# Kernel optimization log

Hardware: AMD Instinct MI355X
Metric: run time of the kernel (lower is better)

The kernel has to match this reference:

```python
import jax, jax.numpy as jnp
import numpy as np

N, E, IN_DIM, HID = 50000, 800000, 512, 256
EPS = 1e-5


def _gat_layer(x, W, a_src, a_dst, b, src, dst, n, heads, ch):
    # x: [N, F_in] -> h: [N, H, C]
    h = (x @ W).reshape(n, heads, ch)
    alpha_src = jnp.sum(h * a_src, axis=-1)  # [N, H]
    alpha_dst = jnp.sum(h * a_dst, axis=-1)  # [N, H]
    e = jax.nn.leaky_relu(alpha_src[src] + alpha_dst[dst], negative_slope=0.2)  # [E', H]
    # segment softmax over incoming edges of each destination node
    m = jax.ops.segment_max(e, dst, num_segments=n)  # [N, H]
    ex = jnp.exp(e - m[dst])
    den = jax.ops.segment_sum(ex, dst, num_segments=n)  # [N, H]
    alpha = ex / den[dst]
    out = jax.ops.segment_sum(alpha[:, :, None] * h[src], dst, num_segments=n)  # [N, H, C]
    return out.reshape(n, heads * ch) + b


def _layer_norm(x, w, b):
    mu = jnp.mean(x, axis=-1, keepdims=True)
    var = jnp.mean(jnp.square(x - mu), axis=-1, keepdims=True)
    return (x - mu) * jax.lax.rsqrt(var + EPS) * w + b


def setup_inputs() -> dict:
    key = jax.random.key(0)
    ks = jax.random.split(key, 16)
    d = {}
    d['x'] = jax.random.normal(ks[0], (N, IN_DIM), dtype=jnp.float32)
    d['edge_index'] = jax.random.randint(ks[1], (2, E), 0, N, dtype=jnp.int32)
    s = 0.05
    # layer 0: GATConv(512, 64, heads=4)
    d['W0'] = jax.random.normal(ks[2], (IN_DIM, HID), dtype=jnp.float32) * s
    d['as0'] = jax.random.normal(ks[3], (4, 64), dtype=jnp.float32) * s
    d['ad0'] = jax.random.normal(ks[4], (4, 64), dtype=jnp.float32) * s
    d['b0'] = jnp.zeros((HID,), dtype=jnp.float32)
    d['lnw0'] = jnp.ones((HID,), dtype=jnp.float32)
    d['lnb0'] = jnp.zeros((HID,), dtype=jnp.float32)
    # layer 1: GATConv(256, 64, heads=4)
    d['W1'] = jax.random.normal(ks[5], (HID, HID), dtype=jnp.float32) * s
    d['as1'] = jax.random.normal(ks[6], (4, 64), dtype=jnp.float32) * s
    d['ad1'] = jax.random.normal(ks[7], (4, 64), dtype=jnp.float32) * s
    d['b1'] = jnp.zeros((HID,), dtype=jnp.float32)
    d['lnw1'] = jnp.ones((HID,), dtype=jnp.float32)
    d['lnb1'] = jnp.zeros((HID,), dtype=jnp.float32)
    # layer 2: GATConv(256, 256, heads=1)
    d['W2'] = jax.random.normal(ks[8], (HID, HID), dtype=jnp.float32) * s
    d['as2'] = jax.random.normal(ks[9], (1, HID), dtype=jnp.float32) * s
    d['ad2'] = jax.random.normal(ks[10], (1, HID), dtype=jnp.float32) * s
    d['b2'] = jnp.zeros((HID,), dtype=jnp.float32)
    d['lnw2'] = jnp.ones((HID,), dtype=jnp.float32)
    d['lnb2'] = jnp.zeros((HID,), dtype=jnp.float32)
    return d


def reference(x, edge_index, W0, as0, ad0, b0, lnw0, lnb0,
              W1, as1, ad1, b1, lnw1, lnb1,
              W2, as2, ad2, b2, lnw2, lnb2):
    n = x.shape[0]
    loop = jnp.arange(n, dtype=edge_index.dtype)
    src = jnp.concatenate([edge_index[0], loop])  # PyG add_self_loops=True
    dst = jnp.concatenate([edge_index[1], loop])
    h = _gat_layer(x, W0, as0, ad0, b0, src, dst, n, 4, 64)
    h = jax.nn.elu(_layer_norm(h, lnw0, lnb0))
    h = _gat_layer(h, W1, as1, ad1, b1, src, dst, n, 4, 64)
    h = jax.nn.elu(_layer_norm(h, lnw1, lnb1))
    h = _gat_layer(h, W2, as2, ad2, b2, src, dst, n, 1, HID)
    h = jax.nn.elu(_layer_norm(h, lnw2, lnb2))
    return h
```

## Files before the change

kernel.cpp:

```cpp
#include <hip/hip_runtime.h>

#define HID 256
#define EPSV 1e-5f
#define ASTR 72
#define BSTR 40

typedef __bf16 bf16x8 __attribute__((ext_vector_type(8)));
typedef float  floatx4 __attribute__((ext_vector_type(4)));

static __device__ __forceinline__ ushort f2bf(float f) {
  union { float f; unsigned int i; } c; c.f = f;
  unsigned int u = c.i;
  u += 0x7FFFu + ((u >> 16) & 1u);
  return (ushort)(u >> 16);
}
static __device__ __forceinline__ float bf2f(ushort u) {
  union { unsigned int i; float f; } c; c.i = ((unsigned int)u) << 16; return c.f;
}

__global__ void count_kernel(const int* __restrict__ ei, int* __restrict__ deg, int E, int tot) {
  int i = blockIdx.x * blockDim.x + threadIdx.x;
  if (i < tot) {
    int dst = (i < E) ? ei[E + i] : (i - E);
    atomicAdd(&deg[dst], 1);
  }
}

__global__ void scanA_kernel(const int* __restrict__ deg, int* __restrict__ incl,
                             int* __restrict__ sums, int n) {
  __shared__ int buf[1024];
  const int t = threadIdx.x;
  const int i = blockIdx.x * 1024 + t;
  int x = (i < n) ? deg[i] : 0;
  buf[t] = x;
  __syncthreads();
  for (int off = 1; off < 1024; off <<= 1) {
    int v = (t >= off) ? buf[t - off] : 0;
    __syncthreads();
    buf[t] += v;
    __syncthreads();
  }
  if (i < n) incl[i] = buf[t];
  if (t == 1023) sums[blockIdx.x] = buf[1023];
}

__global__ void scanB_kernel(int* __restrict__ sums, int* __restrict__ offs, int nblk) {
  __shared__ int buf[256];
  const int t = threadIdx.x;
  int x = (t < nblk) ? sums[t] : 0;
  buf[t] = x;
  __syncthreads();
  for (int off = 1; off < 256; off <<= 1) {
    int v = (t >= off) ? buf[t - off] : 0;
    __syncthreads();
    buf[t] += v;
    __syncthreads();
  }
  if (t < nblk) offs[t] = buf[t] - x;
  if (t == nblk) offs[nblk] = buf[nblk - 1];
}

__global__ void scanC_kernel(const int* __restrict__ deg, const int* __restrict__ incl,
                             const int* __restrict__ offs, int* __restrict__ rp,
                             int* __restrict__ cur, int n, int nblk) {
  const int i = blockIdx.x * 1024 + threadIdx.x;
  if (i < n) {
    int v = offs[blockIdx.x] + incl[i] - deg[i];
    rp[i] = v;
    cur[i] = v;
  }
  if (i == 0) rp[n] = offs[nblk];
}

__global__ void scatter_kernel(const int* __restrict__ ei, int* __restrict__ cur,
                               int* __restrict__ csr, int E, int tot) {
  int i = blockIdx.x * blockDim.x + threadIdx.x;
  if (i < tot) {
    int src = (i < E) ? ei[i] : (i - E);
    int dst = (i < E) ? ei[E + i] : (i - E);
    int pos = atomicAdd(&cur[dst], 1);
    csr[pos] = src;
  }
}

__global__ void transpose_kernel(const float* __restrict__ W, ushort* __restrict__ Wt, int K) {
  int i = blockIdx.x * blockDim.x + threadIdx.x;
  if (i < K * 256) {
    int k = i >> 8, m = i & 255;
    Wt[m * K + k] = f2bf(W[i]);
  }
}

__global__ __launch_bounds__(256) void gemm_kernel(
    const float* __restrict__ A, const ushort* __restrict__ Bt,
    ushort* __restrict__ hb, int nrows, int K) {
  __shared__ ushort At[128 * ASTR];
  __shared__ ushort Bs[128 * BSTR];
  const int tid  = threadIdx.x;
  const int lane = tid & 63;
  const int wave = tid >> 6;
  const int quad = lane >> 4;
  const int m16  = lane & 15;
  const int row0 = blockIdx.x * 128;
  const int col0 = blockIdx.y * 128;
  const int wm = (wave >> 1) * 64;
  const int wn = (wave & 1) * 64;

  floatx4 acc[4][4];
  #pragma unroll
  for (int i = 0; i < 4; i++)
    #pragma unroll
    for (int j = 0; j < 4; j++) acc[i][j] = (floatx4){0.f, 0.f, 0.f, 0.f};

  const int arow = tid >> 3;
  const int acol = (tid & 7) * 4;
  const int brow = tid >> 2;
  const int bcol = (tid & 3) * 8;

  for (int k0 = 0; k0 < K; k0 += 32) {
    #pragma unroll
    for (int i = 0; i < 4; i++) {
      int r = arow + 32 * i;
      int ar = min(row0 + r, nrows - 1);
      floatx4 v = *(const floatx4*)(A + (size_t)ar * K + k0 + acol);
      union { ushort us[4]; unsigned long long u64; } ph, pl;
      #pragma unroll
      for (int j = 0; j < 4; j++) {
        ushort hi = f2bf(v[j]);
        ph.us[j] = hi;
        pl.us[j] = f2bf(v[j] - bf2f(hi));
      }
      *(unsigned long long*)&At[r * ASTR + acol]      = ph.u64;
      *(unsigned long long*)&At[r * ASTR + 32 + acol] = pl.u64;
    }
    #pragma unroll
    for (int i = 0; i < 2; i++) {
      int r = brow + 64 * i;
      *(int4*)&Bs[r * BSTR + bcol] =
          *(const int4*)(Bt + (size_t)(col0 + r) * K + k0 + bcol);
    }
    __syncthreads();
    bf16x8 bfr[4];
    #pragma unroll
    for (int j = 0; j < 4; j++)
      bfr[j] = *(const bf16x8*)&Bs[(wn + j * 16 + m16) * BSTR + quad * 8];
    #pragma unroll
    for (int p = 0; p < 2; p++) {
      bf16x8 af[4];
      #pragma unroll
      for (int i = 0; i < 4; i++)
        af[i] = *(const bf16x8*)&At[(wm + i * 16 + m16) * ASTR + p * 32 + quad * 8];
      #pragma unroll
      for (int i = 0; i < 4; i++)
        #pragma unroll
        for (int j = 0; j < 4; j++)
          acc[i][j] = __builtin_amdgcn_mfma_f32_16x16x32_bf16(af[i], bfr[j], acc[i][j], 0, 0, 0);
    }
    __syncthreads();
  }
  #pragma unroll
  for (int i = 0; i < 4; i++) {
    int rbase = row0 + wm + i * 16 + quad * 4;
    #pragma unroll
    for (int j = 0; j < 4; j++) {
      int col = col0 + wn + j * 16 + m16;
      #pragma unroll
      for (int r = 0; r < 4; r++) {
        int row = rbase + r;
        if (row < nrows) hb[(size_t)row * HID + col] = f2bf(acc[i][j][r]);
      }
    }
  }
}

__global__ __launch_bounds__(256) void gemm_packed_kernel(
    const ushort* __restrict__ A, const ushort* __restrict__ Bt,
    ushort* __restrict__ hb, int nrows) {
  __shared__ ushort At[128 * BSTR];
  __shared__ ushort Bs[128 * BSTR];
  const int tid  = threadIdx.x;
  const int lane = tid & 63;
  const int wave = tid >> 6;
  const int quad = lane >> 4;
  const int m16  = lane & 15;
  const int row0 = blockIdx.x * 128;
  const int col0 = blockIdx.y * 128;
  const int wm = (wave >> 1) * 64;
  const int wn = (wave & 1) * 64;

  floatx4 acc[4][4];
  #pragma unroll
  for (int i = 0; i < 4; i++)
    #pragma unroll
    for (int j = 0; j < 4; j++) acc[i][j] = (floatx4){0.f, 0.f, 0.f, 0.f};

  const int srow = tid >> 2;
  const int scol = (tid & 3) * 8;

  for (int k0 = 0; k0 < 512; k0 += 32) {
    const int kb = k0 & 255;
    #pragma unroll
    for (int i = 0; i < 2; i++) {
      int r = srow + 64 * i;
      int ar = min(row0 + r, nrows - 1);
      *(int4*)&At[r * BSTR + scol] = *(const int4*)(A + (size_t)ar * 512 + k0 + scol);
      *(int4*)&Bs[r * BSTR + scol] = *(const int4*)(Bt + (size_t)(col0 + r) * 256 + kb + scol);
    }
    __syncthreads();
    bf16x8 af[4], bfr[4];
    #pragma unroll
    for (int j = 0; j < 4; j++)
      bfr[j] = *(const bf16x8*)&Bs[(wn + j * 16 + m16) * BSTR + quad * 8];
    #pragma unroll
    for (int i = 0; i < 4; i++)
      af[i] = *(const bf16x8*)&At[(wm + i * 16 + m16) * BSTR + quad * 8];
    #pragma unroll
    for (int i = 0; i < 4; i++)
      #pragma unroll
      for (int j = 0; j < 4; j++)
        acc[i][j] = __builtin_amdgcn_mfma_f32_16x16x32_bf16(af[i], bfr[j], acc[i][j], 0, 0, 0);
    __syncthreads();
  }
  #pragma unroll
  for (int i = 0; i < 4; i++) {
    int rbase = row0 + wm + i * 16 + quad * 4;
    #pragma unroll
    for (int j = 0; j < 4; j++) {
      int col = col0 + wn + j * 16 + m16;
      #pragma unroll
      for (int r = 0; r < 4; r++) {
        int row = rbase + r;
        if (row < nrows) hb[(size_t)row * HID + col] = f2bf(acc[i][j][r]);
      }
    }
  }
}

__global__ __launch_bounds__(256) void alpha_kernel(
    const ushort* __restrict__ hb, const float* __restrict__ avs,
    const float* __restrict__ avd, float* __restrict__ asrc,
    float* __restrict__ adst, int H, int n) {
  const int t = threadIdx.x, w = t >> 6, lane = t & 63;
  const int nid = blockIdx.x * 4 + w;
  if (nid >= n) return;
  const int ch = 4 * lane;
  uint2 hv = *(const uint2*)(hb + (size_t)nid * HID + ch);
  float h0 = __uint_as_float(hv.x << 16);
  float h1 = __uint_as_float(hv.x & 0xffff0000u);
  float h2 = __uint_as_float(hv.y << 16);
  float h3 = __uint_as_float(hv.y & 0xffff0000u);
  floatx4 vs = *(const floatx4*)(avs + ch);
  floatx4 vd = *(const floatx4*)(avd + ch);
  float s = h0 * vs[0] + h1 * vs[1] + h2 * vs[2] + h3 * vs[3];
  float d = h0 * vd[0] + h1 * vd[1] + h2 * vd[2] + h3 * vd[3];
  #pragma unroll
  for (int o = 1; o < 16; o <<= 1) { s += __shfl_xor(s, o); d += __shfl_xor(d, o); }
  if (H == 4) {
    if ((lane & 15) == 0) {
      int hh = lane >> 4;
      asrc[nid * 4 + hh] = s;
      adst[nid * 4 + hh] = d;
    }
  } else {
    s += __shfl_xor(s, 16); d += __shfl_xor(d, 16);
    s += __shfl_xor(s, 32); d += __shfl_xor(d, 32);
    if (lane == 0) { asrc[nid] = s; adst[nid] = d; }
  }
}

__global__ __launch_bounds__(256) void agg_ln_kernel(
    const ushort* __restrict__ hb, const float* __restrict__ asrc,
    const float* __restrict__ adst, const int* __restrict__ rp,
    const int* __restrict__ csr,
    const float* __restrict__ bias, const float* __restrict__ lnw,
    const float* __restrict__ lnb, ushort* __restrict__ apk,
    float* __restrict__ fout, int H, int n) {
  __shared__ float2 exs[4][64];
  const int t = threadIdx.x;
  const int w = t >> 6, lane = t & 63;
  const int nid = blockIdx.x * 4 + w;
  if (nid >= n) return;
  const int CH = (H == 4) ? 16 : 64;
  const int jj = lane & (CH - 1);
  const int hh = (H == 4) ? (lane >> 4) : 0;
  const int ch = 4 * lane;
  const float ad = adst[nid * H + hh];
  const int beg = rp[nid], end = rp[nid + 1];
  const char* hbase = (const char*)hb + ch * 2;
  float den = 0.f;
  float a0 = 0.f, a1 = 0.f, a2 = 0.f, a3 = 0.f;
  float b0 = 0.f, b1 = 0.f, b2 = 0.f, b3 = 0.f;

  for (int c0 = beg; c0 < end; c0 += CH) {
    const int cnt = min(CH, end - c0);
    int s = (lane < cnt) ? csr[c0 + lane] : 0;
    s = __shfl(s, jj);
    float ex = 0.f;
    if (jj < cnt) {
      float e = asrc[s * H + hh] + ad;
      e = (e > 0.f) ? e : 0.2f * e;
      ex = __expf(fminf(e, 60.f));
    }
    exs[w][lane] = make_float2(ex, __int_as_float(s << 9));
    float dsum = ex;
    #pragma unroll
    for (int o = 32; o > 0; o >>= 1)
      if (o < CH) dsum += __shfl_xor(dsum, o);
    den += dsum;
    const float2* exw = &exs[w][hh * CH];
    int j = 0;
    for (; j + 2 <= cnt; j += 2) {
      float2 q0 = exw[j];
      float2 q1 = exw[j + 1];
      uint2 u0 = *(const uint2*)(hbase + __float_as_int(q0.y));
      uint2 u1 = *(const uint2*)(hbase + __float_as_int(q1.y));
      a0 = fmaf(q0.x, __uint_as_float(u0.x << 16), a0);
      a1 = fmaf(q0.x, __uint_as_float(u0.x & 0xffff0000u), a1);
      a2 = fmaf(q0.x, __uint_as_float(u0.y << 16), a2);
      a3 = fmaf(q0.x, __uint_as_float(u0.y & 0xffff0000u), a3);
      b0 = fmaf(q1.x, __uint_as_float(u1.x << 16), b0);
      b1 = fmaf(q1.x, __uint_as_float(u1.x & 0xffff0000u), b1);
      b2 = fmaf(q1.x, __uint_as_float(u1.y << 16), b2);
      b3 = fmaf(q1.x, __uint_as_float(u1.y & 0xffff0000u), b3);
    }
    if (j < cnt) {
      float2 q0 = exw[j];
      uint2 u0 = *(const uint2*)(hbase + __float_as_int(q0.y));
      a0 = fmaf(q0.x, __uint_as_float(u0.x << 16), a0);
      a1 = fmaf(q0.x, __uint_as_float(u0.x & 0xffff0000u), a1);
      a2 = fmaf(q0.x, __uint_as_float(u0.y << 16), a2);
      a3 = fmaf(q0.x, __uint_as_float(u0.y & 0xffff0000u), a3);
    }
  }
  a0 += b0; a1 += b1; a2 += b2; a3 += b3;

  const float inv = 1.f / den;
  const floatx4 bia = *(const floatx4*)(bias + ch);
  float v0 = a0 * inv + bia[0];
  float v1 = a1 * inv + bia[1];
  float v2 = a2 * inv + bia[2];
  float v3 = a3 * inv + bia[3];
  float r1 = v0 + v1 + v2 + v3;
  #pragma unroll
  for (int o = 32; o > 0; o >>= 1) r1 += __shfl_xor(r1, o);
  float mu = r1 * (1.f / HID);
  float d0 = v0 - mu, d1 = v1 - mu, d2 = v2 - mu, d3 = v3 - mu;
  float r2 = d0 * d0 + d1 * d1 + d2 * d2 + d3 * d3;
  #pragma unroll
  for (int o = 32; o > 0; o >>= 1) r2 += __shfl_xor(r2, o);
  float rstd = rsqrtf(r2 * (1.f / HID) + EPSV);
  const floatx4 wv = *(const floatx4*)(lnw + ch);
  const floatx4 bv = *(const floatx4*)(lnb + ch);
  float y0 = d0 * rstd * wv[0] + bv[0];
  float y1 = d1 * rstd * wv[1] + bv[1];
  float y2 = d2 * rstd * wv[2] + bv[2];
  float y3 = d3 * rstd * wv[3] + bv[3];
  float o0 = (y0 > 0.f) ? y0 : expm1f(y0);
  float o1 = (y1 > 0.f) ? y1 : expm1f(y1);
  float o2 = (y2 > 0.f) ? y2 : expm1f(y2);
  float o3 = (y3 > 0.f) ? y3 : expm1f(y3);
  if (apk) {
    union { ushort us[4]; unsigned long long u64; } ph, pl;
    ushort h0 = f2bf(o0), h1 = f2bf(o1), h2 = f2bf(o2), h3 = f2bf(o3);
    ph.us[0] = h0; ph.us[1] = h1; ph.us[2] = h2; ph.us[3] = h3;
    pl.us[0] = f2bf(o0 - bf2f(h0)); pl.us[1] = f2bf(o1 - bf2f(h1));
    pl.us[2] = f2bf(o2 - bf2f(h2)); pl.us[3] = f2bf(o3 - bf2f(h3));
    *(unsigned long long*)(apk + (size_t)nid * 512 + ch)       = ph.u64;
    *(unsigned long long*)(apk + (size_t)nid * 512 + 256 + ch) = pl.u64;
  } else {
    floatx4 ov; ov[0] = o0; ov[1] = o1; ov[2] = o2; ov[3] = o3;
    *(floatx4*)(fout + (size_t)nid * HID + ch) = ov;
  }
}

extern "C" void kernel_launch(void* const* d_in, const int* in_sizes, int n_in,
                              void* d_out, int out_size, void* d_ws, size_t ws_size,
                              hipStream_t stream) {
  const float* x  = (const float*)d_in[0];
  const int*   ei = (const int*)d_in[1];
  const float* Wm[3]  = {(const float*)d_in[2], (const float*)d_in[8],  (const float*)d_in[14]};
  const float* Avs[3] = {(const float*)d_in[3], (const float*)d_in[9],  (const float*)d_in[15]};
  const float* Avd[3] = {(const float*)d_in[4], (const float*)d_in[10], (const float*)d_in[16]};
  const float* Bia[3] = {(const float*)d_in[5], (const float*)d_in[11], (const float*)d_in[17]};
  const float* Lnw[3] = {(const float*)d_in[6], (const float*)d_in[12], (const float*)d_in[18]};
  const float* Lnb[3] = {(const float*)d_in[7], (const float*)d_in[13], (const float*)d_in[19]};
  const int n = in_sizes[0] / 512;
  const int E = in_sizes[1] / 2;
  const int tot = E + n;
  const int nblk = (n + 1023) / 1024;

  char* p = (char*)d_ws;
  ushort* hb   = (ushort*)p; p += (size_t)n * HID * 2;
  ushort* apk  = (ushort*)p; p += (size_t)n * 512 * 2;
  ushort* Wt   = (ushort*)p; p += 256 * 512 * 2;
  float*  asrc = (float*)p;  p += (size_t)n * 4 * 4;
  float*  adst = (float*)p;  p += (size_t)n * 4 * 4;
  int* rp   = (int*)p; p += (size_t)(n + 1) * 4;
  int* cur  = (int*)p; p += (size_t)n * 4;
  int* csr  = (int*)p; p += (size_t)tot * 4;
  int* deg  = (int*)p; p += (size_t)n * 4;
  int* incl = (int*)p; p += (size_t)n * 4;
  int* sums = (int*)p; p += (size_t)(nblk + 1) * 4;
  int* offs = (int*)p; p += (size_t)(nblk + 1) * 4;

  hipMemsetAsync(deg, 0, (size_t)n * 4, stream);
  count_kernel<<<(tot + 255) / 256, 256, 0, stream>>>(ei, deg, E, tot);
  scanA_kernel<<<nblk, 1024, 0, stream>>>(deg, incl, sums, n);
  scanB_kernel<<<1, 256, 0, stream>>>(sums, offs, nblk);
  scanC_kernel<<<nblk, 1024, 0, stream>>>(deg, incl, offs, rp, cur, n, nblk);
  scatter_kernel<<<(tot + 255) / 256, 256, 0, stream>>>(ei, cur, csr, E, tot);

  const int KB[3] = {512, 256, 256};
  const int HH[3] = {4, 4, 1};
  dim3 gg((n + 127) / 128, 2);
  for (int l = 0; l < 3; l++) {
    transpose_kernel<<<(KB[l] * 256 + 255) / 256, 256, 0, stream>>>(Wm[l], Wt, KB[l]);
    if (l == 0)
      gemm_kernel<<<gg, 256, 0, stream>>>(x, Wt, hb, n, 512);
    else
      gemm_packed_kernel<<<gg, 256, 0, stream>>>(apk, Wt, hb, n);
    alpha_kernel<<<(n + 3) / 4, 256, 0, stream>>>(hb, Avs[l], Avd[l], asrc, adst, HH[l], n);
    agg_ln_kernel<<<(n + 3) / 4, 256, 0, stream>>>(
        hb, asrc, adst, rp, csr, Bia[l], Lnw[l], Lnb[l],
        (l < 2) ? apk : (ushort*)nullptr,
        (l == 2) ? (float*)d_out : (float*)nullptr, HH[l], n);
  }
}
```

Before: 640.1 us.

## Fuse attention-logit computation into GEMM epilogue and prefetch/unroll aggregation

Removes the separate alpha kernel by computing per-row source and destination attention logits from the fp32 GEMM accumulators in an epilogue. Heads are reduced with lane shuffles, and the single-head layer combines its partial sums with atomics into zeroed buffers. The aggregation kernel also prefetches the next chunk of CSR indices and unrolls the gather loop four-wide with more independent accumulators. This saves a launch and a re-read of the bf16 features, and the logits now come from unrounded values. In exchange it adds atomics, extra memsets and more register pressure.

Result: no change. 641.7 us (+0.2%).

```diff
diff --git a/kernel.cpp b/kernel.cpp
--- a/kernel.cpp
+++ b/kernel.cpp
@@ -91,9 +91,50 @@
   }
 }
 
+static __device__ __forceinline__ void alpha_epilogue(
+    const floatx4 (&acc)[4][4], const float* __restrict__ avs,
+    const float* __restrict__ avd, float* __restrict__ asrc,
+    float* __restrict__ adst, int row0, int col0, int wm, int wn,
+    int quad, int m16, int H, int nrows) {
+  float sv[4], dv[4];
+  #pragma unroll
+  for (int j = 0; j < 4; j++) {
+    int col = col0 + wn + j * 16 + m16;
+    sv[j] = avs[col];
+    dv[j] = avd[col];
+  }
+  const int hd = (col0 + wn) >> 6;
+  #pragma unroll
+  for (int i = 0; i < 4; i++) {
+    #pragma unroll
+    for (int r = 0; r < 4; r++) {
+      int row = row0 + wm + i * 16 + quad * 4 + r;
+      float s = 0.f, d = 0.f;
+      #pragma unroll
+      for (int j = 0; j < 4; j++) {
+        s = fmaf(acc[i][j][r], sv[j], s);
+        d = fmaf(acc[i][j][r], dv[j], d);
+      }
+      #pragma unroll
+      for (int o = 1; o < 16; o <<= 1) { s += __shfl_xor(s, o); d += __shfl_xor(d, o); }
+      if (m16 == 0 && row < nrows) {
+        if (H == 4) {
+          asrc[row * 4 + hd] = s;
+          adst[row * 4 + hd] = d;
+        } else {
+          atomicAdd(&asrc[row], s);
+          atomicAdd(&adst[row], d);
+        }
+      }
+    }
+  }
+}
+
 __global__ __launch_bounds__(256) void gemm_kernel(
     const float* __restrict__ A, const ushort* __restrict__ Bt,
-    ushort* __restrict__ hb, int nrows, int K) {
+    ushort* __restrict__ hb, const float* __restrict__ avs,
+    const float* __restrict__ avd, float* __restrict__ asrc,
+    float* __restrict__ adst, int nrows, int K) {
   __shared__ ushort At[128 * ASTR];
   __shared__ ushort Bs[128 * BSTR];
   const int tid  = threadIdx.x;
@@ -171,11 +212,14 @@
       }
     }
   }
+  alpha_epilogue(acc, avs, avd, asrc, adst, row0, col0, wm, wn, quad, m16, 4, nrows);
 }
 
 __global__ __launch_bounds__(256) void gemm_packed_kernel(
     const ushort* __restrict__ A, const ushort* __restrict__ Bt,
-    ushort* __restrict__ hb, int nrows) {
+    ushort* __restrict__ hb, const float* __restrict__ avs,
+    const float* __restrict__ avd, float* __restrict__ asrc,
+    float* __restrict__ adst, int nrows, int H) {
   __shared__ ushort At[128 * BSTR];
   __shared__ ushort Bs[128 * BSTR];
   const int tid  = threadIdx.x;
@@ -234,38 +278,7 @@
       }
     }
   }
-}
-
-__global__ __launch_bounds__(256) void alpha_kernel(
-    const ushort* __restrict__ hb, const float* __restrict__ avs,
-    const float* __restrict__ avd, float* __restrict__ asrc,
-    float* __restrict__ adst, int H, int n) {
-  const int t = threadIdx.x, w = t >> 6, lane = t & 63;
-  const int nid = blockIdx.x * 4 + w;
-  if (nid >= n) return;
-  const int ch = 4 * lane;
-  uint2 hv = *(const uint2*)(hb + (size_t)nid * HID + ch);
-  float h0 = __uint_as_float(hv.x << 16);
-  float h1 = __uint_as_float(hv.x & 0xffff0000u);
-  float h2 = __uint_as_float(hv.y << 16);
-  float h3 = __uint_as_float(hv.y & 0xffff0000u);
-  floatx4 vs = *(const floatx4*)(avs + ch);
-  floatx4 vd = *(const floatx4*)(avd + ch);
-  float s = h0 * vs[0] + h1 * vs[1] + h2 * vs[2] + h3 * vs[3];
-  float d = h0 * vd[0] + h1 * vd[1] + h2 * vd[2] + h3 * vd[3];
-  #pragma unroll
-  for (int o = 1; o < 16; o <<= 1) { s += __shfl_xor(s, o); d += __shfl_xor(d, o); }
-  if (H == 4) {
-    if ((lane & 15) == 0) {
-      int hh = lane >> 4;
-      asrc[nid * 4 + hh] = s;
-      adst[nid * 4 + hh] = d;
-    }
-  } else {
-    s += __shfl_xor(s, 16); d += __shfl_xor(d, 16);
-    s += __shfl_xor(s, 32); d += __shfl_xor(d, 32);
-    if (lane == 0) { asrc[nid] = s; adst[nid] = d; }
-  }
+  alpha_epilogue(acc, avs, avd, asrc, adst, row0, col0, wm, wn, quad, m16, H, nrows);
 }
 
 __global__ __launch_bounds__(256) void agg_ln_kernel(
@@ -290,10 +303,23 @@
   float den = 0.f;
   float a0 = 0.f, a1 = 0.f, a2 = 0.f, a3 = 0.f;
   float b0 = 0.f, b1 = 0.f, b2 = 0.f, b3 = 0.f;
+  float c0_ = 0.f, c1 = 0.f, c2 = 0.f, c3 = 0.f;
+  float d0_ = 0.f, d1 = 0.f, d2 = 0.f, d3 = 0.f;
+
+  int snext = 0;
+  {
+    int cnt0 = min(CH, end - beg);
+    if (lane < cnt0) snext = csr[beg + lane];
+  }
 
   for (int c0 = beg; c0 < end; c0 += CH) {
     const int cnt = min(CH, end - c0);
-    int s = (lane < cnt) ? csr[c0 + lane] : 0;
+    int s = snext;
+    const int nc0 = c0 + CH;
+    if (nc0 < end) {
+      int ncnt = min(CH, end - nc0);
+      if (lane < ncnt) snext = csr[nc0 + lane];
+    }
     s = __shfl(s, jj);
     float ex = 0.f;
     if (jj < cnt) {
@@ -309,11 +335,15 @@
     den += dsum;
     const float2* exw = &exs[w][hh * CH];
     int j = 0;
-    for (; j + 2 <= cnt; j += 2) {
+    for (; j + 4 <= cnt; j += 4) {
       float2 q0 = exw[j];
       float2 q1 = exw[j + 1];
+      float2 q2 = exw[j + 2];
+      float2 q3 = exw[j + 3];
       uint2 u0 = *(const uint2*)(hbase + __float_as_int(q0.y));
       uint2 u1 = *(const uint2*)(hbase + __float_as_int(q1.y));
+      uint2 u2 = *(const uint2*)(hbase + __float_as_int(q2.y));
+      uint2 u3 = *(const uint2*)(hbase + __float_as_int(q3.y));
       a0 = fmaf(q0.x, __uint_as_float(u0.x << 16), a0);
       a1 = fmaf(q0.x, __uint_as_float(u0.x & 0xffff0000u), a1);
       a2 = fmaf(q0.x, __uint_as_float(u0.y << 16), a2);
@@ -322,8 +352,16 @@
       b1 = fmaf(q1.x, __uint_as_float(u1.x & 0xffff0000u), b1);
       b2 = fmaf(q1.x, __uint_as_float(u1.y << 16), b2);
       b3 = fmaf(q1.x, __uint_as_float(u1.y & 0xffff0000u), b3);
-    }
-    if (j < cnt) {
+      c0_ = fmaf(q2.x, __uint_as_float(u2.x << 16), c0_);
+      c1 = fmaf(q2.x, __uint_as_float(u2.x & 0xffff0000u), c1);
+      c2 = fmaf(q2.x, __uint_as_float(u2.y << 16), c2);
+      c3 = fmaf(q2.x, __uint_as_float(u2.y & 0xffff0000u), c3);
+      d0_ = fmaf(q3.x, __uint_as_float(u3.x << 16), d0_);
+      d1 = fmaf(q3.x, __uint_as_float(u3.x & 0xffff0000u), d1);
+      d2 = fmaf(q3.x, __uint_as_float(u3.y << 16), d2);
+      d3 = fmaf(q3.x, __uint_as_float(u3.y & 0xffff0000u), d3);
+    }
+    for (; j < cnt; ++j) {
       float2 q0 = exw[j];
       uint2 u0 = *(const uint2*)(hbase + __float_as_int(q0.y));
       a0 = fmaf(q0.x, __uint_as_float(u0.x << 16), a0);
@@ -332,7 +370,10 @@
       a3 = fmaf(q0.x, __uint_as_float(u0.y & 0xffff0000u), a3);
     }
   }
-  a0 += b0; a1 += b1; a2 += b2; a3 += b3;
+  a0 += b0 + c0_ + d0_;
+  a1 += b1 + c1 + d1;
+  a2 += b2 + c2 + d2;
+  a3 += b3 + c3 + d3;
 
   const float inv = 1.f / den;
   const floatx4 bia = *(const floatx4*)(bias + ch);
@@ -344,17 +385,17 @@
   #pragma unroll
   for (int o = 32; o > 0; o >>= 1) r1 += __shfl_xor(r1, o);
   float mu = r1 * (1.f / HID);
-  float d0 = v0 - mu, d1 = v1 - mu, d2 = v2 - mu, d3 = v3 - mu;
-  float r2 = d0 * d0 + d1 * d1 + d2 * d2 + d3 * d3;
+  float e0 = v0 - mu, e1 = v1 - mu, e2 = v2 - mu, e3 = v3 - mu;
+  float r2 = e0 * e0 + e1 * e1 + e2 * e2 + e3 * e3;
   #pragma unroll
   for (int o = 32; o > 0; o >>= 1) r2 += __shfl_xor(r2, o);
   float rstd = rsqrtf(r2 * (1.f / HID) + EPSV);
   const floatx4 wv = *(const floatx4*)(lnw + ch);
   const floatx4 bv = *(const floatx4*)(lnb + ch);
-  float y0 = d0 * rstd * wv[0] + bv[0];
-  float y1 = d1 * rstd * wv[1] + bv[1];
-  float y2 = d2 * rstd * wv[2] + bv[2];
-  float y3 = d3 * rstd * wv[3] + bv[3];
+  float y0 = e0 * rstd * wv[0] + bv[0];
+  float y1 = e1 * rstd * wv[1] + bv[1];
+  float y2 = e2 * rstd * wv[2] + bv[2];
+  float y3 = e3 * rstd * wv[3] + bv[3];
   float o0 = (y0 > 0.f) ? y0 : expm1f(y0);
   float o1 = (y1 > 0.f) ? y1 : expm1f(y1);
   float o2 = (y2 > 0.f) ? y2 : expm1f(y2);
@@ -415,11 +456,14 @@
   dim3 gg((n + 127) / 128, 2);
   for (int l = 0; l < 3; l++) {
     transpose_kernel<<<(KB[l] * 256 + 255) / 256, 256, 0, stream>>>(Wm[l], Wt, KB[l]);
+    if (HH[l] == 1) {
+      hipMemsetAsync(asrc, 0, (size_t)n * 4, stream);
+      hipMemsetAsync(adst, 0, (size_t)n * 4, stream);
+    }
     if (l == 0)
-      gemm_kernel<<<gg, 256, 0, stream>>>(x, Wt, hb, n, 512);
+      gemm_kernel<<<gg, 256, 0, stream>>>(x, Wt, hb, Avs[l], Avd[l], asrc, adst, n, 512);
     else
-      gemm_packed_kernel<<<gg, 256, 0, stream>>>(apk, Wt, hb, n);
-    alpha_kernel<<<(n + 3) / 4, 256, 0, stream>>>(hb, Avs[l], Avd[l], asrc, adst, HH[l], n);
+      gemm_packed_kernel<<<gg, 256, 0, stream>>>(apk, Wt, hb, Avs[l], Avd[l], asrc, adst, n, HH[l]);
     agg_ln_kernel<<<(n + 3) / 4, 256, 0, stream>>>(
         hb, asrc, adst, rp, csr, Bia[l], Lnw[l], Lnb[l],
         (l < 2) ? apk : (ushort*)nullptr,
```
